# Kernel tuning notes

Hardware: AMD Instinct MI355X
Metric: run time of the kernel (lower is better)

The kernel has to match this reference:

```python
import jax, jax.numpy as jnp
import numpy as np

IN_EFF_CORES = 512   # input_vector_size // core_length
IN_CORES = 512
OUT_CORES = 512
SLOTS = 4            # slots_per_core
SLOT_LEN = 64
CONN_P = 0.9
GLOROT = float(np.sqrt(2.0 / (SLOT_LEN + SLOT_LEN)))  # glorot_normal over last two axes


def _make_routing(key, in_cores, out_cores, slots, p):
    """Binary (count) routing tensor C[i,j,k,l]: input core i slot j -> output core k slot l.
    Each output slot samples `slots` sources with replacement, kept with prob p."""
    k1, k2 = jax.random.split(key)
    src = jax.random.randint(k1, (out_cores, slots, slots), 0, in_cores * slots)
    keep = jax.random.bernoulli(k2, p, (out_cores, slots, slots)).astype(jnp.float32)
    oh = jax.nn.one_hot(src, in_cores * slots, dtype=jnp.float32)   # [K,L,R,I*J]
    C = (oh * keep[..., None]).sum(axis=2)                          # [K,L,I*J]
    C = C.reshape(out_cores, slots, in_cores, slots)
    return jnp.transpose(C, (2, 3, 0, 1))                           # [I,J,K,L]


def _act(y, n_states=10, v_max=10.0):
    # capped ReLU: activation(y, 10, 10.0) in the original repo (clipped nonlinearity)
    return jnp.minimum(jax.nn.relu(y), v_max)


def setup_inputs() -> dict:
    key = jax.random.key(0)
    kx, kwi, kwo, kci, kcc = jax.random.split(key, 5)
    x = jax.random.normal(kx, (IN_EFF_CORES * SLOTS * SLOT_LEN,), dtype=jnp.float32)
    Wi = GLOROT * jax.random.normal(kwi, (IN_CORES, SLOTS, SLOTS, SLOT_LEN, SLOT_LEN), dtype=jnp.float32)
    Wo = GLOROT * jax.random.normal(kwo, (OUT_CORES, SLOTS, SLOTS, SLOT_LEN, SLOT_LEN), dtype=jnp.float32)
    Ci = _make_routing(kci, IN_EFF_CORES, IN_CORES, SLOTS, CONN_P)        # [512,4,512,4]
    C_cores = _make_routing(kcc, IN_CORES, OUT_CORES, SLOTS, CONN_P)      # [512,4,512,4]
    return {"x": x, "Wi": Wi, "Wo": Wo, "Ci": Ci, "C_cores": C_cores}


def reference(x, Wi, Wo, Ci, C_cores):
    # x: flat [input_eff_cores*slots*slot_len] -> [I,J,M]
    xr = x.reshape(IN_EFF_CORES, SLOTS, SLOT_LEN)
    # dispatch to input cores: [I,J,K,L] x [I,J,M] -> [K,L,M]
    h = jnp.einsum('ijkl,ijm->klm', Ci, xr)
    # per-core grouped GEMM: [C,J,K,L,M] x [C,K,M] -> [C,J,L]
    y1 = jnp.einsum('ijklm,ikm->ijl', Wi, h)
    y1 = _act(y1)
    # dispatch to output cores
    h2 = jnp.einsum('ijkl,ijm->klm', C_cores, y1)
    y2 = jnp.einsum('ijklm,ikm->ijl', Wo, h2)
    y2 = _act(y2)
    return y2  # [output_cores, slots, slot_len] = [512,4,64]
```

## Files before the change

### kernel.cpp

```cpp
#include <hip/hip_runtime.h>


#define N_CORES 512
#define SLOTS 4
#define SLOT_LEN 64
#define CORE_VEC 256
#define H_ELEMS (N_CORES * CORE_VEC)
#define ROW_LEN 2048

typedef float v4f __attribute__((ext_vector_type(4)));

__device__ __forceinline__ float capped_relu(float v) {
    return fminf(fmaxf(v, 0.0f), 10.0f);
}

__global__ __launch_bounds__(256) void route_src(const float* __restrict__ C,
                                                 const float* __restrict__ src,
                                                 float* __restrict__ h1,
                                                 float* __restrict__ h2) {
    const int gid = blockIdx.x * 256 + threadIdx.x;
    h2[gid] = 0.0f;

    const int wave = blockIdx.x * 4 + (threadIdx.x >> 6);
    const int lane = threadIdx.x & 63;
    const float xv = src[wave * SLOT_LEN + lane];
    const float* row = C + (size_t)wave * ROW_LEN;

    for (int chunk = 0; chunk < 8; ++chunk) {
        v4f c4 = __builtin_nontemporal_load(
            reinterpret_cast<const v4f*>(row) + chunk * 64 + lane);
        #pragma unroll
        for (int q = 0; q < 4; ++q) {
            float cq = c4[q];
            unsigned long long m = __ballot(cq != 0.0f);
            while (m) {
                int L = __ffsll(m) - 1;
                m &= m - 1;
                float c = __shfl(cq, L, 64);
                int dst = chunk * 256 + L * 4 + q;
                atomicAdd(h1 + dst * SLOT_LEN + lane, c * xv);
            }
        }
    }
}

__global__ __launch_bounds__(256) void gemv_route(const float* __restrict__ W,
                                                  const float* __restrict__ h,
                                                  const float* __restrict__ C2,
                                                  float* __restrict__ h2) {
    __shared__ float ly[SLOT_LEN];
    const int i = blockIdx.x >> 2;
    const int j = blockIdx.x & 3;
    const int t = threadIdx.x & 63;
    const int w = threadIdx.x >> 6;
    const int g = t >> 4;
    const int c16 = t & 15;

    const float* row = C2 + (size_t)(i * SLOTS + j) * ROW_LEN;
    v4f cpre[2];
    #pragma unroll
    for (int cc = 0; cc < 2; ++cc)
        cpre[cc] = __builtin_nontemporal_load(
            reinterpret_cast<const v4f*>(row) + (w * 2 + cc) * 64 + t);

    v4f hk[SLOTS];
    #pragma unroll
    for (int k = 0; k < SLOTS; ++k)
        hk[k] = *reinterpret_cast<const v4f*>(h + i * CORE_VEC + k * SLOT_LEN + c16 * 4);

    const float* Wb = W + (size_t)(i * SLOTS + j) * (SLOTS * SLOT_LEN * SLOT_LEN);

    #pragma unroll
    for (int rr = 0; rr < 4; ++rr) {
        const int r = w * 4 + rr;
        float p = 0.0f;
        #pragma unroll
        for (int k = 0; k < SLOTS; ++k) {
            v4f a = __builtin_nontemporal_load(
                reinterpret_cast<const v4f*>(Wb + k * (SLOT_LEN * SLOT_LEN)
                                             + r * 256 + t * 4));
            p += a.x * hk[k].x + a.y * hk[k].y + a.z * hk[k].z + a.w * hk[k].w;
        }
        p += __shfl_xor(p, 1);
        p += __shfl_xor(p, 2);
        p += __shfl_xor(p, 4);
        p += __shfl_xor(p, 8);
        if (c16 == 0) ly[r * 4 + g] = capped_relu(p);
    }
    __syncthreads();

    const float yv = ly[t];
    #pragma unroll
    for (int cc = 0; cc < 2; ++cc) {
        const int chunk = w * 2 + cc;
        #pragma unroll
        for (int q = 0; q < 4; ++q) {
            float cq = cpre[cc][q];
            unsigned long long m = __ballot(cq != 0.0f);
            while (m) {
                int L = __ffsll(m) - 1;
                m &= m - 1;
                float c = __shfl(cq, L, 64);
                int dst = chunk * 256 + L * 4 + q;
                atomicAdd(h2 + dst * SLOT_LEN + t, c * yv);
            }
        }
    }
}

__global__ __launch_bounds__(256) void core_gemv(const float* __restrict__ W,
                                                 const float* __restrict__ h,
                                                 float* __restrict__ out) {
    const int i = blockIdx.x >> 2;
    const int j = blockIdx.x & 3;
    const int t = threadIdx.x & 63;
    const int w = threadIdx.x >> 6;
    const int g = t >> 4;
    const int c16 = t & 15;

    v4f hk[SLOTS];
    #pragma unroll
    for (int k = 0; k < SLOTS; ++k)
        hk[k] = *reinterpret_cast<const v4f*>(h + i * CORE_VEC + k * SLOT_LEN + c16 * 4);

    const float* Wb = W + (size_t)(i * SLOTS + j) * (SLOTS * SLOT_LEN * SLOT_LEN);

    #pragma unroll
    for (int rr = 0; rr < 4; ++rr) {
        const int r = w * 4 + rr;
        float p = 0.0f;
        #pragma unroll
        for (int k = 0; k < SLOTS; ++k) {
            v4f a = __builtin_nontemporal_load(
                reinterpret_cast<const v4f*>(Wb + k * (SLOT_LEN * SLOT_LEN)
                                             + r * 256 + t * 4));
            p += a.x * hk[k].x + a.y * hk[k].y + a.z * hk[k].z + a.w * hk[k].w;
        }
        p += __shfl_xor(p, 1);
        p += __shfl_xor(p, 2);
        p += __shfl_xor(p, 4);
        p += __shfl_xor(p, 8);
        if (c16 == 0)
            out[(i * SLOTS + j) * SLOT_LEN + r * 4 + g] = capped_relu(p);
    }
}

extern "C" void kernel_launch(void* const* d_in, const int* in_sizes, int n_in,
                              void* d_out, int out_size, void* d_ws, size_t ws_size,
                              hipStream_t stream) {
    const float* x  = (const float*)d_in[0];
    const float* Wi = (const float*)d_in[1];
    const float* Wo = (const float*)d_in[2];
    const float* Ci = (const float*)d_in[3];
    const float* Cc = (const float*)d_in[4];
    float* out = (float*)d_out;

    float* h1 = (float*)d_ws;
    float* h2 = h1 + H_ELEMS;

    hipMemsetAsync(h1, 0, H_ELEMS * sizeof(float), stream);

    route_src<<<512, 256, 0, stream>>>(Ci, x, h1, h2);
    gemv_route<<<2048, 256, 0, stream>>>(Wi, h1, Cc, h2);
    core_gemv<<<2048, 256, 0, stream>>>(Wo, h2, out);
}
```

Before: 292.7 us.

## Fuse memset and three stages into one cooperative kernel with grid syncs

Replaces the memset and the three separate launches (routing, first grouped GEMV plus routing, second grouped GEMV) with one cooperative kernel of 512 blocks. Grid-wide syncs separate the phases, and each block now handles all four slots of a core serially instead of one slot per block. This removes launch and memset overhead but cuts parallelism from 2048 to 512 blocks in the GEMV phases. That may leave memory-bound weight streaming with less latency hiding, and it adds the cost of the grid syncs.

```diff
diff --git a/kernel.cpp b/kernel.cpp
--- a/kernel.cpp
+++ b/kernel.cpp
@@ -1,4 +1,7 @@
 #include <hip/hip_runtime.h>
+#include <hip/hip_cooperative_groups.h>
+
+namespace cg = cooperative_groups;
 
 
 #define N_CORES 512
@@ -7,6 +10,7 @@
 #define CORE_VEC 256
 #define H_ELEMS (N_CORES * CORE_VEC)
 #define ROW_LEN 2048
+#define W_CORE (SLOTS * SLOT_LEN * SLOT_LEN)
 
 typedef float v4f __attribute__((ext_vector_type(4)));
 
@@ -14,134 +18,135 @@
     return fminf(fmaxf(v, 0.0f), 10.0f);
 }
 
-__global__ __launch_bounds__(256) void route_src(const float* __restrict__ C,
-                                                 const float* __restrict__ src,
-                                                 float* __restrict__ h1,
-                                                 float* __restrict__ h2) {
-    const int gid = blockIdx.x * 256 + threadIdx.x;
+__global__ __launch_bounds__(256, 2) void fused(
+        const float* __restrict__ x,
+        const float* __restrict__ Wi,
+        const float* __restrict__ Wo,
+        const float* __restrict__ Ci,
+        const float* __restrict__ Cc,
+        float* __restrict__ h1,
+        float* __restrict__ h2,
+        float* __restrict__ out) {
+    cg::grid_group grid = cg::this_grid();
+
+    const int b   = blockIdx.x;
+    const int tid = threadIdx.x;
+    const int t   = tid & 63;
+    const int w   = tid >> 6;
+    const int g   = t >> 4;
+    const int c16 = t & 15;
+
+    __shared__ float ly[SLOT_LEN];
+
+    const int gid = b * 256 + tid;
+    h1[gid] = 0.0f;
     h2[gid] = 0.0f;
+    grid.sync();
 
-    const int wave = blockIdx.x * 4 + (threadIdx.x >> 6);
-    const int lane = threadIdx.x & 63;
-    const float xv = src[wave * SLOT_LEN + lane];
-    const float* row = C + (size_t)wave * ROW_LEN;
-
-    for (int chunk = 0; chunk < 8; ++chunk) {
-        v4f c4 = __builtin_nontemporal_load(
-            reinterpret_cast<const v4f*>(row) + chunk * 64 + lane);
-        #pragma unroll
-        for (int q = 0; q < 4; ++q) {
-            float cq = c4[q];
-            unsigned long long m = __ballot(cq != 0.0f);
-            while (m) {
-                int L = __ffsll(m) - 1;
-                m &= m - 1;
-                float c = __shfl(cq, L, 64);
-                int dst = chunk * 256 + L * 4 + q;
-                atomicAdd(h1 + dst * SLOT_LEN + lane, c * xv);
+    {
+        const int row_id = b * SLOTS + w;
+        const float xv = x[row_id * SLOT_LEN + t];
+        const v4f* row4 = reinterpret_cast<const v4f*>(Ci + (size_t)row_id * ROW_LEN);
+        for (int chunk = 0; chunk < 8; ++chunk) {
+            v4f c4 = __builtin_nontemporal_load(row4 + chunk * 64 + t);
+            #pragma unroll
+            for (int q = 0; q < 4; ++q) {
+                float cq = c4[q];
+                unsigned long long m = __ballot(cq != 0.0f);
+                while (m) {
+                    int L = __ffsll(m) - 1;
+                    m &= m - 1;
+                    float c = __shfl(cq, L, 64);
+                    int dst = chunk * 256 + L * 4 + q;
+                    atomicAdd(h1 + dst * SLOT_LEN + t, c * xv);
+                }
             }
         }
     }
-}
+    grid.sync();
 
-__global__ __launch_bounds__(256) void gemv_route(const float* __restrict__ W,
-                                                  const float* __restrict__ h,
-                                                  const float* __restrict__ C2,
-                                                  float* __restrict__ h2) {
-    __shared__ float ly[SLOT_LEN];
-    const int i = blockIdx.x >> 2;
-    const int j = blockIdx.x & 3;
-    const int t = threadIdx.x & 63;
-    const int w = threadIdx.x >> 6;
-    const int g = t >> 4;
-    const int c16 = t & 15;
+    {
+        v4f hk[SLOTS];
+        #pragma unroll
+        for (int k = 0; k < SLOTS; ++k)
+            hk[k] = *reinterpret_cast<const v4f*>(h1 + b * CORE_VEC + k * SLOT_LEN + c16 * 4);
 
-    const float* row = C2 + (size_t)(i * SLOTS + j) * ROW_LEN;
-    v4f cpre[2];
-    #pragma unroll
-    for (int cc = 0; cc < 2; ++cc)
-        cpre[cc] = __builtin_nontemporal_load(
-            reinterpret_cast<const v4f*>(row) + (w * 2 + cc) * 64 + t);
+        for (int j = 0; j < SLOTS; ++j) {
+            const int p = b * SLOTS + j;
+            const v4f* row4 = reinterpret_cast<const v4f*>(Cc + (size_t)p * ROW_LEN);
+            v4f cpre[2];
+            #pragma unroll
+            for (int cc = 0; cc < 2; ++cc)
+                cpre[cc] = __builtin_nontemporal_load(row4 + (w * 2 + cc) * 64 + t);
 
-    v4f hk[SLOTS];
-    #pragma unroll
-    for (int k = 0; k < SLOTS; ++k)
-        hk[k] = *reinterpret_cast<const v4f*>(h + i * CORE_VEC + k * SLOT_LEN + c16 * 4);
+            const float* Wb = Wi + (size_t)p * W_CORE;
+            #pragma unroll
+            for (int rr = 0; rr < 4; ++rr) {
+                const int r = w * 4 + rr;
+                float pacc = 0.0f;
+                #pragma unroll
+                for (int k = 0; k < SLOTS; ++k) {
+                    v4f a = __builtin_nontemporal_load(
+                        reinterpret_cast<const v4f*>(Wb + k * (SLOT_LEN * SLOT_LEN)
+                                                     + r * 256 + t * 4));
+                    pacc += a.x * hk[k].x + a.y * hk[k].y + a.z * hk[k].z + a.w * hk[k].w;
+                }
+                pacc += __shfl_xor(pacc, 1);
+                pacc += __shfl_xor(pacc, 2);
+                pacc += __shfl_xor(pacc, 4);
+                pacc += __shfl_xor(pacc, 8);
+                if (c16 == 0) ly[r * 4 + g] = capped_relu(pacc);
+            }
+            __syncthreads();
+            const float yv = ly[t];
+            #pragma unroll
+            for (int cc = 0; cc < 2; ++cc) {
+                const int chunk = w * 2 + cc;
+                #pragma unroll
+                for (int q = 0; q < 4; ++q) {
+                    float cq = cpre[cc][q];
+                    unsigned long long m = __ballot(cq != 0.0f);
+                    while (m) {
+                        int L = __ffsll(m) - 1;
+                        m &= m - 1;
+                        float c = __shfl(cq, L, 64);
+                        int dst = chunk * 256 + L * 4 + q;
+                        atomicAdd(h2 + dst * SLOT_LEN + t, c * yv);
+                    }
+                }
+            }
+            __syncthreads();
+        }
+    }
+    grid.sync();
 
-    const float* Wb = W + (size_t)(i * SLOTS + j) * (SLOTS * SLOT_LEN * SLOT_LEN);
+    {
+        v4f hk[SLOTS];
+        #pragma unroll
+        for (int k = 0; k < SLOTS; ++k)
+            hk[k] = *reinterpret_cast<const v4f*>(h2 + b * CORE_VEC + k * SLOT_LEN + c16 * 4);
 
-    #pragma unroll
-    for (int rr = 0; rr < 4; ++rr) {
-        const int r = w * 4 + rr;
-        float p = 0.0f;
-        #pragma unroll
-        for (int k = 0; k < SLOTS; ++k) {
-            v4f a = __builtin_nontemporal_load(
-                reinterpret_cast<const v4f*>(Wb + k * (SLOT_LEN * SLOT_LEN)
-                                             + r * 256 + t * 4));
-            p += a.x * hk[k].x + a.y * hk[k].y + a.z * hk[k].z + a.w * hk[k].w;
-        }
-        p += __shfl_xor(p, 1);
-        p += __shfl_xor(p, 2);
-        p += __shfl_xor(p, 4);
-        p += __shfl_xor(p, 8);
-        if (c16 == 0) ly[r * 4 + g] = capped_relu(p);
-    }
-    __syncthreads();
-
-    const float yv = ly[t];
-    #pragma unroll
-    for (int cc = 0; cc < 2; ++cc) {
-        const int chunk = w * 2 + cc;
-        #pragma unroll
-        for (int q = 0; q < 4; ++q) {
-            float cq = cpre[cc][q];
-            unsigned long long m = __ballot(cq != 0.0f);
-            while (m) {
-                int L = __ffsll(m) - 1;
-                m &= m - 1;
-                float c = __shfl(cq, L, 64);
-                int dst = chunk * 256 + L * 4 + q;
-                atomicAdd(h2 + dst * SLOT_LEN + t, c * yv);
+        for (int j = 0; j < SLOTS; ++j) {
+            const float* Wb = Wo + (size_t)(b * SLOTS + j) * W_CORE;
+            #pragma unroll
+            for (int rr = 0; rr < 4; ++rr) {
+                const int r = w * 4 + rr;
+                float pacc = 0.0f;
+                #pragma unroll
+                for (int k = 0; k < SLOTS; ++k) {
+                    v4f a = __builtin_nontemporal_load(
+                        reinterpret_cast<const v4f*>(Wb + k * (SLOT_LEN * SLOT_LEN)
+                                                     + r * 256 + t * 4));
+                    pacc += a.x * hk[k].x + a.y * hk[k].y + a.z * hk[k].z + a.w * hk[k].w;
+                }
+                pacc += __shfl_xor(pacc, 1);
+                pacc += __shfl_xor(pacc, 2);
+                pacc += __shfl_xor(pacc, 4);
+                pacc += __shfl_xor(pacc, 8);
+                if (c16 == 0)
+                    out[(b * SLOTS + j) * SLOT_LEN + r * 4 + g] = capped_relu(pacc);
             }
         }
-    }
-}
-
-__global__ __launch_bounds__(256) void core_gemv(const float* __restrict__ W,
-                                                 const float* __restrict__ h,
-                                                 float* __restrict__ out) {
-    const int i = blockIdx.x >> 2;
-    const int j = blockIdx.x & 3;
-    const int t = threadIdx.x & 63;
-    const int w = threadIdx.x >> 6;
-    const int g = t >> 4;
-    const int c16 = t & 15;
-
-    v4f hk[SLOTS];
-    #pragma unroll
-    for (int k = 0; k < SLOTS; ++k)
-        hk[k] = *reinterpret_cast<const v4f*>(h + i * CORE_VEC + k * SLOT_LEN + c16 * 4);
-
-    const float* Wb = W + (size_t)(i * SLOTS + j) * (SLOTS * SLOT_LEN * SLOT_LEN);
-
-    #pragma unroll
-    for (int rr = 0; rr < 4; ++rr) {
-        const int r = w * 4 + rr;
-        float p = 0.0f;
-        #pragma unroll
-        for (int k = 0; k < SLOTS; ++k) {
-            v4f a = __builtin_nontemporal_load(
-                reinterpret_cast<const v4f*>(Wb + k * (SLOT_LEN * SLOT_LEN)
-                                             + r * 256 + t * 4));
-            p += a.x * hk[k].x + a.y * hk[k].y + a.z * hk[k].z + a.w * hk[k].w;
-        }
-        p += __shfl_xor(p, 1);
-        p += __shfl_xor(p, 2);
-        p += __shfl_xor(p, 4);
-        p += __shfl_xor(p, 8);
-        if (c16 == 0)
-            out[(i * SLOTS + j) * SLOT_LEN + r * 4 + g] = capped_relu(p);
     }
 }
 
@@ -158,9 +163,7 @@
     float* h1 = (float*)d_ws;
     float* h2 = h1 + H_ELEMS;
 
-    hipMemsetAsync(h1, 0, H_ELEMS * sizeof(float), stream);
-
-    route_src<<<512, 256, 0, stream>>>(Ci, x, h1, h2);
-    gemv_route<<<2048, 256, 0, stream>>>(Wi, h1, Cc, h2);
-    core_gemv<<<2048, 256, 0, stream>>>(Wo, h2, out);
+    void* args[] = {(void*)&x, (void*)&Wi, (void*)&Wo, (void*)&Ci, (void*)&Cc,
+                    (void*)&h1, (void*)&h2, (void*)&out};
+    hipLaunchCooperativeKernel((void*)fused, dim3(512), dim3(256), args, 0, stream);
 }
```

Measured after the change: 458.2 us. +56.5%, slower.
